# Kernel tuning notes

Measured on AMD Instinct MI355X. Metric: run time of the kernel, lower is better.

## Reference

```python
import jax, jax.numpy as jnp
import numpy as np

WS = 8          # window_size
HEADS = 6
DH = 32         # dim_head


def _dwconv(t, w):
    # t: (B,C,H,W), w: (C,1,3,3) depthwise, stride 1, padding 1 -> SAME
    return jax.lax.conv_general_dilated(
        t, w, window_strides=(1, 1), padding='SAME',
        feature_group_count=t.shape[1],
        dimension_numbers=('NCHW', 'OIHW', 'NCHW'))


def _l2norm(t, eps=1e-12):
    # matches F.normalize: x / max(||x||, eps)
    n = jnp.sqrt(jnp.sum(t * t, axis=-1, keepdims=True))
    return t / jnp.maximum(n, eps)


def setup_inputs() -> dict:
    key = jax.random.key(0)
    ks = jax.random.split(key, 10)
    B, H, W, C = 2, 256, 256, 192
    s = 0.05
    return {
        'x': jax.random.normal(ks[0], (B, H, W, C), jnp.float32),
        'illu_fea_trans': jax.random.normal(ks[1], (B, H, W, C), jnp.float32),
        'gt_w': jax.random.normal(ks[2], (C, C), jnp.float32) * s,
        'gt_b': jax.random.normal(ks[3], (C,), jnp.float32) * s,
        'qkv_w': jax.random.normal(ks[4], (C, 3 * C), jnp.float32) * s,
        'qkv_b': jax.random.normal(ks[5], (3 * C,), jnp.float32) * s,
        'proj_w': jax.random.normal(ks[6], (C, C), jnp.float32) * s,
        'proj_b': jax.random.normal(ks[7], (C,), jnp.float32) * s,
        'conv1_w': jax.random.normal(ks[8], (C, 1, 3, 3), jnp.float32) * s,
        'conv2_w': jax.random.normal(ks[9], (C, 1, 3, 3), jnp.float32) * s,
    }


def reference(x, illu_fea_trans, gt_w, gt_b, qkv_w, qkv_b, proj_w, proj_b,
              conv1_w, conv2_w):
    B, H, W, C = x.shape
    Ws, heads, d = WS, HEADS, DH
    scale = d ** (-0.5)
    pad_h = (Ws - H % Ws) % Ws
    pad_w = (Ws - W % Ws) % Ws
    xp = jnp.pad(x, ((0, 0), (0, pad_h), (0, pad_w), (0, 0)), mode='reflect')
    ip = jnp.pad(illu_fea_trans, ((0, 0), (0, pad_h), (0, pad_w), (0, 0)), mode='reflect')
    Hp, Wp = xp.shape[1], xp.shape[2]
    nW = (Hp // Ws) * (Wp // Ws)
    T = Ws * Ws

    def to_windows(t):
        t = t.reshape(B, Hp // Ws, Ws, Wp // Ws, Ws, C)
        return t.transpose(0, 1, 3, 2, 4, 5).reshape(B * nW, T, C)

    xw = to_windows(xp)                                  # (B*nW, T, C)
    qkv = (xw @ qkv_w + qkv_b).reshape(B * nW, T, 3, heads, d)
    qkv = qkv.transpose(2, 0, 3, 1, 4)                   # (3, Bn, h, T, d)
    q, k, v = qkv[0], qkv[1], qkv[2]
    q = _l2norm(q)
    k = _l2norm(k)

    illu = to_windows(ip).reshape(B * nW, T, heads, d).transpose(0, 2, 1, 3)
    v = v * (1.0 + jax.nn.sigmoid(illu))

    # global token: avg-pool over padded spatial dims, then linear
    gt = jnp.mean(xp, axis=(1, 2)) @ gt_w + gt_b          # (B, C)
    gt = gt.reshape(B, heads, 1, d)
    # faithful to torch expand(dim=2 -> nW).reshape(B*nW, heads, 1, d)
    gk = jnp.broadcast_to(gt, (B, heads, nW, d)).reshape(B * nW, heads, 1, d)
    k = jnp.concatenate([k, gk], axis=2)                  # (Bn, h, T+1, d)
    v = jnp.concatenate([v, gk], axis=2)

    # chunked softmax over keys == full softmax over key axis (chunks on q only)
    attn = jax.nn.softmax(jnp.einsum('bhqd,bhkd->bhqk', q, k) * scale, axis=-1)
    out = jnp.einsum('bhqk,bhkd->bhqd', attn, v)          # (Bn, h, T, d)
    out = out.transpose(0, 2, 1, 3).reshape(B * nW, T, C)
    out = out @ proj_w + proj_b

    out = out.reshape(B, Hp // Ws, Wp // Ws, Ws, Ws, C)
    out = out.transpose(0, 1, 3, 2, 4, 5).reshape(B, Hp, Wp, C)[:, :H, :W, :]

    # depthwise-conv positional branch on padded x (exact gelu like torch)
    t = xp.transpose(0, 3, 1, 2)                          # (B,C,Hp,Wp)
    t = _dwconv(t, conv1_w)
    t = jax.nn.gelu(t, approximate=False)
    t = _dwconv(t, conv2_w)
    pos = t.transpose(0, 2, 3, 1)[:, :H, :W, :]
    return out + pos
```

## Files before the change

### kernel.cpp

```cpp
#include <hip/hip_runtime.h>
#include <hip/hip_bf16.h>

#define BB   2
#define HH   256
#define WWD  256
#define CC   192
#define WSZ  8
#define TT   64
#define NHD  6
#define DHD  32
#define N3   576

typedef __attribute__((ext_vector_type(8))) short short8;
typedef __attribute__((ext_vector_type(4))) float f32x4;

__device__ inline short bf16_bits(float f) {
  __hip_bfloat16 h = __float2bfloat16(f);
  return __builtin_bit_cast(short, h);
}

__device__ inline float row_sum16(float v) {
  int x;
  x = __builtin_amdgcn_update_dpp(0, __builtin_bit_cast(int, v), 0xB1, 0xf, 0xf, true);
  v += __builtin_bit_cast(float, x);
  x = __builtin_amdgcn_update_dpp(0, __builtin_bit_cast(int, v), 0x4E, 0xf, 0xf, true);
  v += __builtin_bit_cast(float, x);
  x = __builtin_amdgcn_update_dpp(0, __builtin_bit_cast(int, v), 0x124, 0xf, 0xf, true);
  v += __builtin_bit_cast(float, x);
  x = __builtin_amdgcn_update_dpp(0, __builtin_bit_cast(int, v), 0x128, 0xf, 0xf, true);
  v += __builtin_bit_cast(float, x);
  return v;
}

__device__ inline void stage1k(const short* gsrc, short* ldst, int lane) {
  __builtin_amdgcn_global_load_lds(
      (const __attribute__((address_space(1))) void*)(gsrc + lane * 8),
      (__attribute__((address_space(3))) void*)ldst, 16, 0, 0);
}

__global__ __launch_bounds__(256) void lcam_wshuf2(const float* __restrict__ qkv_w,
                                                   const float* __restrict__ proj_w,
                                                   short* __restrict__ wf,
                                                   short* __restrict__ pwf) {
  int gid = blockIdx.x * 256 + threadIdx.x;
  const float* src; short* dst; int ncols, perm, g;
  if (gid < 13824) { src = qkv_w; dst = wf; ncols = N3; perm = 0; g = gid; }
  else {
    g = gid - 13824;
    if (g >= 4608) return;
    src = proj_w; dst = pwf; ncols = CC; perm = 1;
  }
  int lane = g & 63;
  int s = (g >> 6) % 6;
  int ct = g / 384;
  int col = ct * 16 + (lane & 15);
  int k0 = s * 32 + (lane >> 4) * 8;
  short8 v;
#pragma unroll
  for (int j = 0; j < 8; ++j)
    v[j] = bf16_bits(src[(size_t)(k0 + j) * ncols + col]);
  int didx = perm ? ((s * (ncols / 16) + ct) * 64 + lane) : g;
  *(short8*)(dst + (size_t)didx * 8) = v;
}

__global__ __launch_bounds__(192) void lcam_sum_x(const float* __restrict__ x,
                                                  float* __restrict__ sums) {
  int blk = blockIdx.x;
  int b = blk >> 9;
  int chunk = blk & 511;
  const float4* xp = (const float4*)(x + ((size_t)b * 65536 + (size_t)chunk * 128) * CC);
  int t = threadIdx.x;
  int pg = t / 48, c4 = t % 48;
  float4 acc = {0.f, 0.f, 0.f, 0.f};
  for (int p = 0; p < 32; ++p) {
    float4 v = xp[(size_t)(pg * 32 + p) * 48 + c4];
    acc.x += v.x; acc.y += v.y; acc.z += v.z; acc.w += v.w;
  }
  __shared__ __align__(16) float4 red[192];
  red[t] = acc;
  __syncthreads();
  if (pg == 0) {
    float4 a0 = red[c4], a1 = red[48 + c4], a2 = red[96 + c4], a3 = red[144 + c4];
    float* s = &sums[b * CC + c4 * 4];
    atomicAdd(s + 0, a0.x + a1.x + a2.x + a3.x);
    atomicAdd(s + 1, a0.y + a1.y + a2.y + a3.y);
    atomicAdd(s + 2, a0.z + a1.z + a2.z + a3.z);
    atomicAdd(s + 3, a0.w + a1.w + a2.w + a3.w);
  }
}

__global__ void lcam_gt(const float* __restrict__ sums,
                        const float* __restrict__ gt_w,
                        const float* __restrict__ gt_b,
                        float* __restrict__ gt) {
  int b = blockIdx.x;
  int co = threadIdx.x;
  float acc = gt_b[co];
  const float inv = 1.f / 65536.f;
  for (int c = 0; c < CC; ++c)
    acc += sums[b * CC + c] * inv * gt_w[c * CC + co];
  gt[b * CC + co] = acc;
}

__global__ __launch_bounds__(256) void lcam_attn(
    const float* __restrict__ x, const float* __restrict__ illu,
    const short* __restrict__ wf, const short* __restrict__ pwf,
    const float* __restrict__ qkv_b, const float* __restrict__ proj_b,
    const float* __restrict__ gt, float* __restrict__ out) {
  __shared__ __align__(16) short wgt[2][6144];
  __shared__ __align__(16) short ks[65 * 40];
  __shared__ __align__(16) short vt[32 * 72];
  __shared__ __align__(16) short qs[64 * 40];
  __shared__ __align__(16) short ps[64 * 72];

  int w = blockIdx.x;
  int b  = w >> 10;
  int wy = (w >> 5) & 31;
  int wx = w & 31;
  int t  = threadIdx.x;
  int lane = t & 63;
  int rtile = t >> 6;
  int m = lane & 15;
  int quad = lane >> 4;
  int key0 = rtile * 16 + quad * 4;

  size_t base = ((size_t)(b * HH + wy * WSZ) * WWD + wx * WSZ) * CC;

#pragma unroll
  for (int u = 0; u < 3; ++u) {
    int ii = rtile * 3 + u;
    stage1k(wf + ii * 512, wgt[0] + ii * 512, lane);
  }

  int apix = rtile * 16 + m;
  size_t arow = base + (size_t)((apix >> 3) * WWD + (apix & 7)) * CC + quad * 8;
  short8 afrag[6];
#pragma unroll
  for (int s = 0; s < 6; ++s) {
    const float* ap = x + arow + s * 32;
    float4 f0 = *(const float4*)(ap);
    float4 f1 = *(const float4*)(ap + 4);
    short8 v;
    v[0] = bf16_bits(f0.x); v[1] = bf16_bits(f0.y);
    v[2] = bf16_bits(f0.z); v[3] = bf16_bits(f0.w);
    v[4] = bf16_bits(f1.x); v[5] = bf16_bits(f1.y);
    v[6] = bf16_bits(f1.z); v[7] = bf16_bits(f1.w);
    afrag[s] = v;
  }

  float ila[NHD][4], ilb[NHD][4];
#pragma unroll
  for (int r = 0; r < 4; ++r) {
    int key = key0 + r;
    const float* ip = illu + base + (size_t)((key >> 3) * WWD + (key & 7)) * CC;
#pragma unroll
    for (int h = 0; h < NHD; ++h) {
      ila[h][r] = ip[h * 32 + m];
      ilb[h][r] = ip[h * 32 + 16 + m];
    }
  }

  const short8* wA8 = (const short8*)wgt[0];
  const short8* wB8 = (const short8*)wgt[1];

  f32x4 pacc[12];
#pragma unroll
  for (int ct = 0; ct < 12; ++ct) {
    f32x4 z = {0.f, 0.f, 0.f, 0.f};
    pacc[ct] = z;
  }

  __syncthreads();

#pragma unroll
  for (int h = 0; h < NHD; ++h) {
#pragma unroll
    for (int u = 0; u < 3; ++u) {
      int ii = rtile * 3 + u;
      stage1k(wf + (12 + 2 * h) * 3072 + ii * 512, wgt[1] + ii * 512, lane);
    }
    float gv0 = gt[b * CC + h * 32 + m];
    float gv1 = gt[b * CC + h * 32 + 16 + m];
    {
      f32x4 a0 = {0.f,0.f,0.f,0.f}, a1 = {0.f,0.f,0.f,0.f};
      __builtin_amdgcn_s_setprio(1);
#pragma unroll
      for (int s = 0; s < 6; ++s)
        a0 = __builtin_amdgcn_mfma_f32_16x16x32_bf16(afrag[s], wA8[s*64 + lane], a0, 0,0,0);
#pragma unroll
      for (int s = 0; s < 6; ++s)
        a1 = __builtin_amdgcn_mfma_f32_16x16x32_bf16(afrag[s], wA8[384 + s*64 + lane], a1, 0,0,0);
      __builtin_amdgcn_s_setprio(0);
      float b0 = qkv_b[h*32 + m], b1 = qkv_b[h*32 + 16 + m];
#pragma unroll
      for (int r = 0; r < 4; ++r) {
        float v0 = a0[r] + b0, v1 = a1[r] + b1;
        float ss = row_sum16(v0*v0 + v1*v1);
        float scl = 0.17677669529663688f * __builtin_amdgcn_rsqf(fmaxf(ss, 1e-24f));
        int row = key0 + r;
        qs[row*40 + m]      = bf16_bits(v0 * scl);
        qs[row*40 + 16 + m] = bf16_bits(v1 * scl);
      }
    }
    __syncthreads();
#pragma unroll
    for (int u = 0; u < 3; ++u) {
      int ii = rtile * 3 + u;
      stage1k(wf + (24 + 2 * h) * 3072 + ii * 512, wgt[0] + ii * 512, lane);
    }
    {
      f32x4 a0 = {0.f,0.f,0.f,0.f}, a1 = {0.f,0.f,0.f,0.f};
      __builtin_amdgcn_s_setprio(1);
#pragma unroll
      for (int s = 0; s < 6; ++s)
        a0 = __builtin_amdgcn_mfma_f32_16x16x32_bf16(afrag[s], wB8[s*64 + lane], a0, 0,0,0);
#pragma unroll
      for (int s = 0; s < 6; ++s)
        a1 = __builtin_amdgcn_mfma_f32_16x16x32_bf16(afrag[s], wB8[384 + s*64 + lane], a1, 0,0,0);
      __builtin_amdgcn_s_setprio(0);
      float b0 = qkv_b[192 + h*32 + m], b1 = qkv_b[192 + h*32 + 16 + m];
#pragma unroll
      for (int r = 0; r < 4; ++r) {
        float v0 = a0[r] + b0, v1 = a1[r] + b1;
        float ss = row_sum16(v0*v0 + v1*v1);
        float scl = __builtin_amdgcn_rsqf(fmaxf(ss, 1e-24f));
        int row = key0 + r;
        ks[row*40 + m]      = bf16_bits(v0 * scl);
        ks[row*40 + 16 + m] = bf16_bits(v1 * scl);
      }
    }
    __syncthreads();
#pragma unroll
    for (int u = 0; u < 3; ++u) {
      int ii = rtile * 3 + u;
      stage1k(pwf + h * 6144 + ii * 512, wgt[1] + ii * 512, lane);
    }
    {
      f32x4 a0 = {0.f,0.f,0.f,0.f}, a1 = {0.f,0.f,0.f,0.f};
      __builtin_amdgcn_s_setprio(1);
#pragma unroll
      for (int s = 0; s < 6; ++s)
        a0 = __builtin_amdgcn_mfma_f32_16x16x32_bf16(afrag[s], wA8[s*64 + lane], a0, 0,0,0);
#pragma unroll
      for (int s = 0; s < 6; ++s)
        a1 = __builtin_amdgcn_mfma_f32_16x16x32_bf16(afrag[s], wA8[384 + s*64 + lane], a1, 0,0,0);
      __builtin_amdgcn_s_setprio(0);
      float b0 = qkv_b[384 + h*32 + m], b1 = qkv_b[384 + h*32 + 16 + m];
#pragma unroll
      for (int r = 0; r < 4; ++r) {
        int key = key0 + r;
        float s0 = __builtin_amdgcn_rcpf(1.f + __expf(-ila[h][r]));
        float s1 = __builtin_amdgcn_rcpf(1.f + __expf(-ilb[h][r]));
        vt[m*72 + key]        = bf16_bits((a0[r] + b0) * (1.f + s0));
        vt[(16 + m)*72 + key] = bf16_bits((a1[r] + b1) * (1.f + s1));
      }
    }
    if (t < DHD) ks[64*40 + t] = bf16_bits(gt[b*CC + h*DHD + t]);
    __syncthreads();
    if (h < NHD - 1) {
#pragma unroll
      for (int u = 0; u < 3; ++u) {
        int ii = rtile * 3 + u;
        stage1k(wf + 2 * (h + 1) * 3072 + ii * 512, wgt[0] + ii * 512, lane);
      }
    }
    short8 qa = *(const short8*)(qs + (rtile*16 + m)*40 + quad*8);
    f32x4 sc[5];
#pragma unroll
    for (int ct = 0; ct < 4; ++ct) {
      short8 kb = *(const short8*)(ks + (ct*16 + m)*40 + quad*8);
      f32x4 z = {0.f,0.f,0.f,0.f};
      sc[ct] = __builtin_amdgcn_mfma_f32_16x16x32_bf16(qa, kb, z, 0,0,0);
    }
    {
      short8 kb = *(const short8*)(ks + 64*40 + quad*8);
      f32x4 z = {0.f,0.f,0.f,0.f};
      sc[4] = __builtin_amdgcn_mfma_f32_16x16x32_bf16(qa, kb, z, 0,0,0);
    }
    float p64v[4], invr[4];
#pragma unroll
    for (int r = 0; r < 4; ++r) {
      float e0 = __expf(sc[0][r]), e1 = __expf(sc[1][r]);
      float e2 = __expf(sc[2][r]), e3 = __expf(sc[3][r]);
      float e4 = __expf(sc[4][r]);
      int row = key0 + r;
      ps[row*72 + m]      = bf16_bits(e0);
      ps[row*72 + 16 + m] = bf16_bits(e1);
      ps[row*72 + 32 + m] = bf16_bits(e2);
      ps[row*72 + 48 + m] = bf16_bits(e3);
      float sum = row_sum16(e0 + e1 + e2 + e3) + e4;
      invr[r] = __builtin_amdgcn_rcpf(sum);
      p64v[r] = e4;
    }
    f32x4 o0 = {0.f,0.f,0.f,0.f}, o1 = {0.f,0.f,0.f,0.f};
    __builtin_amdgcn_s_setprio(1);
#pragma unroll
    for (int kc = 0; kc < 2; ++kc) {
      short8 pa  = *(const short8*)(ps + (rtile*16 + m)*72 + kc*32 + quad*8);
      short8 vb0 = *(const short8*)(vt + m*72        + kc*32 + quad*8);
      short8 vb1 = *(const short8*)(vt + (16 + m)*72 + kc*32 + quad*8);
      o0 = __builtin_amdgcn_mfma_f32_16x16x32_bf16(pa, vb0, o0, 0,0,0);
      o1 = __builtin_amdgcn_mfma_f32_16x16x32_bf16(pa, vb1, o1, 0,0,0);
    }
    __builtin_amdgcn_s_setprio(0);
#pragma unroll
    for (int r = 0; r < 4; ++r) {
      float pr = p64v[r];
      int row = key0 + r;
      qs[row*40 + m]      = bf16_bits((o0[r] + pr * gv0) * invr[r]);
      qs[row*40 + 16 + m] = bf16_bits((o1[r] + pr * gv1) * invr[r]);
    }
    short8 oa = *(const short8*)(qs + (rtile*16 + m)*40 + quad*8);
    __builtin_amdgcn_s_setprio(1);
#pragma unroll
    for (int ct = 0; ct < 12; ++ct)
      pacc[ct] = __builtin_amdgcn_mfma_f32_16x16x32_bf16(oa, wB8[ct*64 + lane], pacc[ct], 0,0,0);
    __builtin_amdgcn_s_setprio(0);
    __syncthreads();
  }
#pragma unroll
  for (int ct = 0; ct < 12; ++ct) {
    float bias = proj_b[ct*16 + m];
#pragma unroll
    for (int r = 0; r < 4; ++r) {
      int row = key0 + r;
      out[base + (size_t)((row >> 3) * WWD + (row & 7)) * CC + ct*16 + m] = pacc[ct][r] + bias;
    }
  }
}

__global__ __launch_bounds__(256) void lcam_pos(const float* __restrict__ x,
                                                const float* __restrict__ w1,
                                                const float* __restrict__ w2,
                                                float* __restrict__ out) {
  __shared__ __align__(16) float xt[20 * 20 * 16];
  __shared__ __align__(16) float t1[18 * 18 * 16];
  __shared__ float wl1[16 * 9], wl2[16 * 9];
  int blk = blockIdx.x;
  int cgI = blk % 12; int tmp = blk / 12;
  int tx = tmp % 16; tmp /= 16;
  int ty = tmp % 16; int b = tmp / 16;
  int c0 = cgI * 16;
  int y0 = ty * 16, x0 = tx * 16;
  int t = threadIdx.x;
  int cc4 = t & 3;
  if (t < 144) { wl1[t] = w1[c0 * 9 + t]; wl2[t] = w2[c0 * 9 + t]; }
  for (int vi = t; vi < 1600; vi += 256) {
    int q4 = vi & 3;
    int lin = vi >> 2;
    int xx = lin % 20, yy = lin / 20;
    int gy = y0 - 2 + yy, gx = x0 - 2 + xx;
    float4 v = {0.f, 0.f, 0.f, 0.f};
    if (gy >= 0 && gy < HH && gx >= 0 && gx < WWD)
      v = *(const float4*)(x + (((size_t)b * HH + gy) * WWD + gx) * CC + c0 + q4 * 4);
    *(float4*)(xt + (yy * 20 + xx) * 16 + q4 * 4) = v;
  }
  __syncthreads();
  float w1r[4][9], w2r[4][9];
#pragma unroll
  for (int j = 0; j < 4; ++j)
#pragma unroll
    for (int k = 0; k < 9; ++k) {
      w1r[j][k] = wl1[(cc4 * 4 + j) * 9 + k];
      w2r[j][k] = wl2[(cc4 * 4 + j) * 9 + k];
    }
  for (int idx = t; idx < 1296; idx += 256) {
    int lin = idx >> 2;
    int xx = lin % 18, yy = lin / 18;
    int gy = y0 - 1 + yy, gx = x0 - 1 + xx;
    float4 r = {0.f, 0.f, 0.f, 0.f};
    if (gy >= 0 && gy < HH && gx >= 0 && gx < WWD) {
#pragma unroll
      for (int ky = 0; ky < 3; ++ky)
#pragma unroll
        for (int kx = 0; kx < 3; ++kx) {
          float4 v = *(const float4*)(xt + ((yy + ky) * 20 + xx + kx) * 16 + cc4 * 4);
          int k = ky * 3 + kx;
          r.x += v.x * w1r[0][k];
          r.y += v.y * w1r[1][k];
          r.z += v.z * w1r[2][k];
          r.w += v.w * w1r[3][k];
        }
      r.x = 0.5f * r.x * (1.f + erff(r.x * 0.70710678118654752f));
      r.y = 0.5f * r.y * (1.f + erff(r.y * 0.70710678118654752f));
      r.z = 0.5f * r.z * (1.f + erff(r.z * 0.70710678118654752f));
      r.w = 0.5f * r.w * (1.f + erff(r.w * 0.70710678118654752f));
    }
    *(float4*)(t1 + (yy * 18 + xx) * 16 + cc4 * 4) = r;
  }
  __syncthreads();
  for (int idx = t; idx < 1024; idx += 256) {
    int lin = idx >> 2;
    int xx = lin & 15, yy = lin >> 4;
    float4 r = {0.f, 0.f, 0.f, 0.f};
#pragma unroll
    for (int ky = 0; ky < 3; ++ky)
#pragma unroll
      for (int kx = 0; kx < 3; ++kx) {
        float4 v = *(const float4*)(t1 + ((yy + ky) * 18 + xx + kx) * 16 + cc4 * 4);
        int k = ky * 3 + kx;
        r.x += v.x * w2r[0][k];
        r.y += v.y * w2r[1][k];
        r.z += v.z * w2r[2][k];
        r.w += v.w * w2r[3][k];
      }
    size_t o = (((size_t)b * HH + y0 + yy) * WWD + x0 + xx) * CC + c0 + cc4 * 4;
    float4 cur = *(float4*)(out + o);
    cur.x += r.x; cur.y += r.y; cur.z += r.z; cur.w += r.w;
    *(float4*)(out + o) = cur;
  }
}

extern "C" void kernel_launch(void* const* d_in, const int* in_sizes, int n_in,
                              void* d_out, int out_size, void* d_ws, size_t ws_size,
                              hipStream_t stream) {
  const float* x       = (const float*)d_in[0];
  const float* illu    = (const float*)d_in[1];
  const float* gt_w    = (const float*)d_in[2];
  const float* gt_b    = (const float*)d_in[3];
  const float* qkv_w   = (const float*)d_in[4];
  const float* qkv_b   = (const float*)d_in[5];
  const float* proj_w  = (const float*)d_in[6];
  const float* proj_b  = (const float*)d_in[7];
  const float* conv1_w = (const float*)d_in[8];
  const float* conv2_w = (const float*)d_in[9];
  float* out = (float*)d_out;

  short* wf   = (short*)d_ws;
  short* pwf  = (short*)((char*)d_ws + 221184);
  float* sums = (float*)((char*)d_ws + 221184 + 73728);
  float* gt   = sums + BB * CC;

  hipMemsetAsync(sums, 0, BB * CC * sizeof(float), stream);
  lcam_wshuf2<<<72, 256, 0, stream>>>(qkv_w, proj_w, wf, pwf);
  lcam_sum_x<<<1024, 192, 0, stream>>>(x, sums);
  lcam_gt<<<BB, CC, 0, stream>>>(sums, gt_w, gt_b, gt);
  lcam_attn<<<2048, 256, 0, stream>>>(x, illu, wf, pwf, qkv_b, proj_b, gt, out);
  lcam_pos<<<6144, 256, 0, stream>>>(x, conv1_w, conv2_w, out);
}
```

Before: 523.0 us.

## Process two windows per block, each wave handling two row tiles

Each 256-thread block now handles two attention windows instead of one. Each wave computes two 16-row tiles and reuses each weight fragment read from shared memory for two MFMAs. This halves the block count, and with it the number of times each block stages the full QKV and projection weights into LDS. It also halves the weight LDS reads per MFMA. The illumination loads move into the head loop. The cost is doubled accumulator registers (two sets of 12 projection accumulators plus the extra fragments), which could lower occupancy or cause spills. The per-window LDS buffers also double.

```diff
diff --git a/kernel.cpp b/kernel.cpp
--- a/kernel.cpp
+++ b/kernel.cpp
@@ -108,66 +108,69 @@
     const float* __restrict__ qkv_b, const float* __restrict__ proj_b,
     const float* __restrict__ gt, float* __restrict__ out) {
   __shared__ __align__(16) short wgt[2][6144];
-  __shared__ __align__(16) short ks[65 * 40];
-  __shared__ __align__(16) short vt[32 * 72];
-  __shared__ __align__(16) short qs[64 * 40];
-  __shared__ __align__(16) short ps[64 * 72];
-
-  int w = blockIdx.x;
-  int b  = w >> 10;
-  int wy = (w >> 5) & 31;
-  int wx = w & 31;
-  int t  = threadIdx.x;
+  __shared__ __align__(16) short ks[2][65 * 40];
+  __shared__ __align__(16) short vt[2][32 * 72];
+  __shared__ __align__(16) short qs[2][64 * 40];
+  __shared__ __align__(16) short ps[2][64 * 72];
+
+  int t = threadIdx.x;
   int lane = t & 63;
-  int rtile = t >> 6;
+  int wid = t >> 6;
+  int win = wid >> 1;
+  int half = wid & 1;
   int m = lane & 15;
   int quad = lane >> 4;
-  int key0 = rtile * 16 + quad * 4;
-
+  int tl = t & 127;
+
+  int wA = blockIdx.x * 2 + win;
+  int b  = wA >> 10;
+  int wy = (wA >> 5) & 31;
+  int wx = wA & 31;
   size_t base = ((size_t)(b * HH + wy * WSZ) * WWD + wx * WSZ) * CC;
 
+  short* ksb = ks[win];
+  short* vtb = vt[win];
+  short* qsb = qs[win];
+  short* psb = ps[win];
+
+  int rb0 = half * 32;
+  int rb1 = half * 32 + 16;
+  int key00 = rb0 + quad * 4;
+  int key01 = rb1 + quad * 4;
+
 #pragma unroll
   for (int u = 0; u < 3; ++u) {
-    int ii = rtile * 3 + u;
+    int ii = wid * 3 + u;
     stage1k(wf + ii * 512, wgt[0] + ii * 512, lane);
   }
 
-  int apix = rtile * 16 + m;
-  size_t arow = base + (size_t)((apix >> 3) * WWD + (apix & 7)) * CC + quad * 8;
-  short8 afrag[6];
-#pragma unroll
-  for (int s = 0; s < 6; ++s) {
-    const float* ap = x + arow + s * 32;
-    float4 f0 = *(const float4*)(ap);
-    float4 f1 = *(const float4*)(ap + 4);
-    short8 v;
-    v[0] = bf16_bits(f0.x); v[1] = bf16_bits(f0.y);
-    v[2] = bf16_bits(f0.z); v[3] = bf16_bits(f0.w);
-    v[4] = bf16_bits(f1.x); v[5] = bf16_bits(f1.y);
-    v[6] = bf16_bits(f1.z); v[7] = bf16_bits(f1.w);
-    afrag[s] = v;
-  }
-
-  float ila[NHD][4], ilb[NHD][4];
-#pragma unroll
-  for (int r = 0; r < 4; ++r) {
-    int key = key0 + r;
-    const float* ip = illu + base + (size_t)((key >> 3) * WWD + (key & 7)) * CC;
-#pragma unroll
-    for (int h = 0; h < NHD; ++h) {
-      ila[h][r] = ip[h * 32 + m];
-      ilb[h][r] = ip[h * 32 + 16 + m];
+  short8 af0[6], af1[6];
+#pragma unroll
+  for (int g = 0; g < 2; ++g) {
+    int apix = (g ? rb1 : rb0) + m;
+    size_t arow = base + (size_t)((apix >> 3) * WWD + (apix & 7)) * CC + quad * 8;
+#pragma unroll
+    for (int s = 0; s < 6; ++s) {
+      const float* ap = x + arow + s * 32;
+      float4 f0 = *(const float4*)(ap);
+      float4 f1 = *(const float4*)(ap + 4);
+      short8 v;
+      v[0] = bf16_bits(f0.x); v[1] = bf16_bits(f0.y);
+      v[2] = bf16_bits(f0.z); v[3] = bf16_bits(f0.w);
+      v[4] = bf16_bits(f1.x); v[5] = bf16_bits(f1.y);
+      v[6] = bf16_bits(f1.z); v[7] = bf16_bits(f1.w);
+      if (g) af1[s] = v; else af0[s] = v;
     }
   }
 
   const short8* wA8 = (const short8*)wgt[0];
   const short8* wB8 = (const short8*)wgt[1];
 
-  f32x4 pacc[12];
+  f32x4 pacc0[12], pacc1[12];
 #pragma unroll
   for (int ct = 0; ct < 12; ++ct) {
     f32x4 z = {0.f, 0.f, 0.f, 0.f};
-    pacc[ct] = z;
+    pacc0[ct] = z; pacc1[ct] = z;
   }
 
   __syncthreads();
@@ -176,145 +179,215 @@
   for (int h = 0; h < NHD; ++h) {
 #pragma unroll
     for (int u = 0; u < 3; ++u) {
-      int ii = rtile * 3 + u;
+      int ii = wid * 3 + u;
       stage1k(wf + (12 + 2 * h) * 3072 + ii * 512, wgt[1] + ii * 512, lane);
     }
     float gv0 = gt[b * CC + h * 32 + m];
     float gv1 = gt[b * CC + h * 32 + 16 + m];
+    float il00[4], il01[4], il10[4], il11[4];
+#pragma unroll
+    for (int r = 0; r < 4; ++r) {
+      int k0r = key00 + r, k1r = key01 + r;
+      const float* ip0 = illu + base + (size_t)((k0r >> 3) * WWD + (k0r & 7)) * CC + h * 32;
+      const float* ip1 = illu + base + (size_t)((k1r >> 3) * WWD + (k1r & 7)) * CC + h * 32;
+      il00[r] = ip0[m]; il01[r] = ip0[16 + m];
+      il10[r] = ip1[m]; il11[r] = ip1[16 + m];
+    }
     {
-      f32x4 a0 = {0.f,0.f,0.f,0.f}, a1 = {0.f,0.f,0.f,0.f};
+      f32x4 a00 = {0.f,0.f,0.f,0.f}, a01 = {0.f,0.f,0.f,0.f};
+      f32x4 a10 = {0.f,0.f,0.f,0.f}, a11 = {0.f,0.f,0.f,0.f};
       __builtin_amdgcn_s_setprio(1);
 #pragma unroll
-      for (int s = 0; s < 6; ++s)
-        a0 = __builtin_amdgcn_mfma_f32_16x16x32_bf16(afrag[s], wA8[s*64 + lane], a0, 0,0,0);
-#pragma unroll
-      for (int s = 0; s < 6; ++s)
-        a1 = __builtin_amdgcn_mfma_f32_16x16x32_bf16(afrag[s], wA8[384 + s*64 + lane], a1, 0,0,0);
+      for (int s = 0; s < 6; ++s) {
+        short8 w0 = wA8[s*64 + lane];
+        a00 = __builtin_amdgcn_mfma_f32_16x16x32_bf16(af0[s], w0, a00, 0,0,0);
+        a10 = __builtin_amdgcn_mfma_f32_16x16x32_bf16(af1[s], w0, a10, 0,0,0);
+      }
+#pragma unroll
+      for (int s = 0; s < 6; ++s) {
+        short8 w1 = wA8[384 + s*64 + lane];
+        a01 = __builtin_amdgcn_mfma_f32_16x16x32_bf16(af0[s], w1, a01, 0,0,0);
+        a11 = __builtin_amdgcn_mfma_f32_16x16x32_bf16(af1[s], w1, a11, 0,0,0);
+      }
       __builtin_amdgcn_s_setprio(0);
       float b0 = qkv_b[h*32 + m], b1 = qkv_b[h*32 + 16 + m];
 #pragma unroll
       for (int r = 0; r < 4; ++r) {
-        float v0 = a0[r] + b0, v1 = a1[r] + b1;
+        float v0 = a00[r] + b0, v1 = a01[r] + b1;
         float ss = row_sum16(v0*v0 + v1*v1);
         float scl = 0.17677669529663688f * __builtin_amdgcn_rsqf(fmaxf(ss, 1e-24f));
-        int row = key0 + r;
-        qs[row*40 + m]      = bf16_bits(v0 * scl);
-        qs[row*40 + 16 + m] = bf16_bits(v1 * scl);
+        int row = key00 + r;
+        qsb[row*40 + m]      = bf16_bits(v0 * scl);
+        qsb[row*40 + 16 + m] = bf16_bits(v1 * scl);
+        float w0 = a10[r] + b0, w1 = a11[r] + b1;
+        float ss1 = row_sum16(w0*w0 + w1*w1);
+        float scl1 = 0.17677669529663688f * __builtin_amdgcn_rsqf(fmaxf(ss1, 1e-24f));
+        int row1 = key01 + r;
+        qsb[row1*40 + m]      = bf16_bits(w0 * scl1);
+        qsb[row1*40 + 16 + m] = bf16_bits(w1 * scl1);
       }
     }
     __syncthreads();
 #pragma unroll
     for (int u = 0; u < 3; ++u) {
-      int ii = rtile * 3 + u;
+      int ii = wid * 3 + u;
       stage1k(wf + (24 + 2 * h) * 3072 + ii * 512, wgt[0] + ii * 512, lane);
     }
     {
-      f32x4 a0 = {0.f,0.f,0.f,0.f}, a1 = {0.f,0.f,0.f,0.f};
+      f32x4 a00 = {0.f,0.f,0.f,0.f}, a01 = {0.f,0.f,0.f,0.f};
+      f32x4 a10 = {0.f,0.f,0.f,0.f}, a11 = {0.f,0.f,0.f,0.f};
       __builtin_amdgcn_s_setprio(1);
 #pragma unroll
-      for (int s = 0; s < 6; ++s)
-        a0 = __builtin_amdgcn_mfma_f32_16x16x32_bf16(afrag[s], wB8[s*64 + lane], a0, 0,0,0);
-#pragma unroll
-      for (int s = 0; s < 6; ++s)
-        a1 = __builtin_amdgcn_mfma_f32_16x16x32_bf16(afrag[s], wB8[384 + s*64 + lane], a1, 0,0,0);
+      for (int s = 0; s < 6; ++s) {
+        short8 w0 = wB8[s*64 + lane];
+        a00 = __builtin_amdgcn_mfma_f32_16x16x32_bf16(af0[s], w0, a00, 0,0,0);
+        a10 = __builtin_amdgcn_mfma_f32_16x16x32_bf16(af1[s], w0, a10, 0,0,0);
+      }
+#pragma unroll
+      for (int s = 0; s < 6; ++s) {
+        short8 w1 = wB8[384 + s*64 + lane];
+        a01 = __builtin_amdgcn_mfma_f32_16x16x32_bf16(af0[s], w1, a01, 0,0,0);
+        a11 = __builtin_amdgcn_mfma_f32_16x16x32_bf16(af1[s], w1, a11, 0,0,0);
+      }
       __builtin_amdgcn_s_setprio(0);
       float b0 = qkv_b[192 + h*32 + m], b1 = qkv_b[192 + h*32 + 16 + m];
 #pragma unroll
       for (int r = 0; r < 4; ++r) {
-        float v0 = a0[r] + b0, v1 = a1[r] + b1;
+        float v0 = a00[r] + b0, v1 = a01[r] + b1;
         float ss = row_sum16(v0*v0 + v1*v1);
         float scl = __builtin_amdgcn_rsqf(fmaxf(ss, 1e-24f));
-        int row = key0 + r;
-        ks[row*40 + m]      = bf16_bits(v0 * scl);
-        ks[row*40 + 16 + m] = bf16_bits(v1 * scl);
+        int row = key00 + r;
+        ksb[row*40 + m]      = bf16_bits(v0 * scl);
+        ksb[row*40 + 16 + m] = bf16_bits(v1 * scl);
+        float w0 = a10[r] + b0, w1 = a11[r] + b1;
+        float ss1 = row_sum16(w0*w0 + w1*w1);
+        float scl1 = __builtin_amdgcn_rsqf(fmaxf(ss1, 1e-24f));
+        int row1 = key01 + r;
+        ksb[row1*40 + m]      = bf16_bits(w0 * scl1);
+        ksb[row1*40 + 16 + m] = bf16_bits(w1 * scl1);
       }
     }
     __syncthreads();
 #pragma unroll
     for (int u = 0; u < 3; ++u) {
-      int ii = rtile * 3 + u;
+      int ii = wid * 3 + u;
       stage1k(pwf + h * 6144 + ii * 512, wgt[1] + ii * 512, lane);
     }
     {
-      f32x4 a0 = {0.f,0.f,0.f,0.f}, a1 = {0.f,0.f,0.f,0.f};
+      f32x4 a00 = {0.f,0.f,0.f,0.f}, a01 = {0.f,0.f,0.f,0.f};
+      f32x4 a10 = {0.f,0.f,0.f,0.f}, a11 = {0.f,0.f,0.f,0.f};
       __builtin_amdgcn_s_setprio(1);
 #pragma unroll
-      for (int s = 0; s < 6; ++s)
-        a0 = __builtin_amdgcn_mfma_f32_16x16x32_bf16(afrag[s], wA8[s*64 + lane], a0, 0,0,0);
-#pragma unroll
-      for (int s = 0; s < 6; ++s)
-        a1 = __builtin_amdgcn_mfma_f32_16x16x32_bf16(afrag[s], wA8[384 + s*64 + lane], a1, 0,0,0);
+      for (int s = 0; s < 6; ++s) {
+        short8 w0 = wA8[s*64 + lane];
+        a00 = __builtin_amdgcn_mfma_f32_16x16x32_bf16(af0[s], w0, a00, 0,0,0);
+        a10 = __builtin_amdgcn_mfma_f32_16x16x32_bf16(af1[s], w0, a10, 0,0,0);
+      }
+#pragma unroll
+      for (int s = 0; s < 6; ++s) {
+        short8 w1 = wA8[384 + s*64 + lane];
+        a01 = __builtin_amdgcn_mfma_f32_16x16x32_bf16(af0[s], w1, a01, 0,0,0);
+        a11 = __builtin_amdgcn_mfma_f32_16x16x32_bf16(af1[s], w1, a11, 0,0,0);
+      }
       __builtin_amdgcn_s_setprio(0);
       float b0 = qkv_b[384 + h*32 + m], b1 = qkv_b[384 + h*32 + 16 + m];
 #pragma unroll
       for (int r = 0; r < 4; ++r) {
-        int key = key0 + r;
-        float s0 = __builtin_amdgcn_rcpf(1.f + __expf(-ila[h][r]));
-        float s1 = __builtin_amdgcn_rcpf(1.f + __expf(-ilb[h][r]));
-        vt[m*72 + key]        = bf16_bits((a0[r] + b0) * (1.f + s0));
-        vt[(16 + m)*72 + key] = bf16_bits((a1[r] + b1) * (1.f + s1));
-      }
-    }
-    if (t < DHD) ks[64*40 + t] = bf16_bits(gt[b*CC + h*DHD + t]);
+        int k0r = key00 + r, k1r = key01 + r;
+        float s00 = __builtin_amdgcn_rcpf(1.f + __expf(-il00[r]));
+        float s01 = __builtin_amdgcn_rcpf(1.f + __expf(-il01[r]));
+        float s10 = __builtin_amdgcn_rcpf(1.f + __expf(-il10[r]));
+        float s11 = __builtin_amdgcn_rcpf(1.f + __expf(-il11[r]));
+        vtb[m*72 + k0r]        = bf16_bits((a00[r] + b0) * (1.f + s00));
+        vtb[(16 + m)*72 + k0r] = bf16_bits((a01[r] + b1) * (1.f + s01));
+        vtb[m*72 + k1r]        = bf16_bits((a10[r] + b0) * (1.f + s10));
+        vtb[(16 + m)*72 + k1r] = bf16_bits((a11[r] + b1) * (1.f + s11));
+      }
+    }
+    if (tl < DHD) ksb[64*40 + tl] = bf16_bits(gt[b*CC + h*DHD + tl]);
     __syncthreads();
     if (h < NHD - 1) {
 #pragma unroll
       for (int u = 0; u < 3; ++u) {
-        int ii = rtile * 3 + u;
+        int ii = wid * 3 + u;
         stage1k(wf + 2 * (h + 1) * 3072 + ii * 512, wgt[0] + ii * 512, lane);
       }
     }
-    short8 qa = *(const short8*)(qs + (rtile*16 + m)*40 + quad*8);
-    f32x4 sc[5];
+    short8 qa0 = *(const short8*)(qsb + (rb0 + m)*40 + quad*8);
+    short8 qa1 = *(const short8*)(qsb + (rb1 + m)*40 + quad*8);
+    f32x4 sc0[5], sc1[5];
+    __builtin_amdgcn_s_setprio(1);
 #pragma unroll
     for (int ct = 0; ct < 4; ++ct) {
-      short8 kb = *(const short8*)(ks + (ct*16 + m)*40 + quad*8);
+      short8 kb = *(const short8*)(ksb + (ct*16 + m)*40 + quad*8);
       f32x4 z = {0.f,0.f,0.f,0.f};
-      sc[ct] = __builtin_amdgcn_mfma_f32_16x16x32_bf16(qa, kb, z, 0,0,0);
+      sc0[ct] = __builtin_amdgcn_mfma_f32_16x16x32_bf16(qa0, kb, z, 0,0,0);
+      sc1[ct] = __builtin_amdgcn_mfma_f32_16x16x32_bf16(qa1, kb, z, 0,0,0);
     }
     {
-      short8 kb = *(const short8*)(ks + 64*40 + quad*8);
+      short8 kb = *(const short8*)(ksb + 64*40 + quad*8);
       f32x4 z = {0.f,0.f,0.f,0.f};
-      sc[4] = __builtin_amdgcn_mfma_f32_16x16x32_bf16(qa, kb, z, 0,0,0);
-    }
-    float p64v[4], invr[4];
+      sc0[4] = __builtin_amdgcn_mfma_f32_16x16x32_bf16(qa0, kb, z, 0,0,0);
+      sc1[4] = __builtin_amdgcn_mfma_f32_16x16x32_bf16(qa1, kb, z, 0,0,0);
+    }
+    __builtin_amdgcn_s_setprio(0);
+    float p640[4], inv0[4], p641[4], inv1[4];
 #pragma unroll
     for (int r = 0; r < 4; ++r) {
-      float e0 = __expf(sc[0][r]), e1 = __expf(sc[1][r]);
-      float e2 = __expf(sc[2][r]), e3 = __expf(sc[3][r]);
-      float e4 = __expf(sc[4][r]);
-      int row = key0 + r;
-      ps[row*72 + m]      = bf16_bits(e0);
-      ps[row*72 + 16 + m] = bf16_bits(e1);
-      ps[row*72 + 32 + m] = bf16_bits(e2);
-      ps[row*72 + 48 + m] = bf16_bits(e3);
-      float sum = row_sum16(e0 + e1 + e2 + e3) + e4;
-      invr[r] = __builtin_amdgcn_rcpf(sum);
-      p64v[r] = e4;
-    }
-    f32x4 o0 = {0.f,0.f,0.f,0.f}, o1 = {0.f,0.f,0.f,0.f};
+      float e0 = __expf(sc0[0][r]), e1 = __expf(sc0[1][r]);
+      float e2 = __expf(sc0[2][r]), e3 = __expf(sc0[3][r]);
+      float e4 = __expf(sc0[4][r]);
+      int row = key00 + r;
+      psb[row*72 + m]      = bf16_bits(e0);
+      psb[row*72 + 16 + m] = bf16_bits(e1);
+      psb[row*72 + 32 + m] = bf16_bits(e2);
+      psb[row*72 + 48 + m] = bf16_bits(e3);
+      inv0[r] = __builtin_amdgcn_rcpf(row_sum16(e0 + e1 + e2 + e3) + e4);
+      p640[r] = e4;
+      float f0 = __expf(sc1[0][r]), f1 = __expf(sc1[1][r]);
+      float f2 = __expf(sc1[2][r]), f3 = __expf(sc1[3][r]);
+      float f4 = __expf(sc1[4][r]);
+      int row1 = key01 + r;
+      psb[row1*72 + m]      = bf16_bits(f0);
+      psb[row1*72 + 16 + m] = bf16_bits(f1);
+      psb[row1*72 + 32 + m] = bf16_bits(f2);
+      psb[row1*72 + 48 + m] = bf16_bits(f3);
+      inv1[r] = __builtin_amdgcn_rcpf(row_sum16(f0 + f1 + f2 + f3) + f4);
+      p641[r] = f4;
+    }
+    f32x4 o00 = {0.f,0.f,0.f,0.f}, o01 = {0.f,0.f,0.f,0.f};
+    f32x4 o10 = {0.f,0.f,0.f,0.f}, o11 = {0.f,0.f,0.f,0.f};
     __builtin_amdgcn_s_setprio(1);
 #pragma unroll
     for (int kc = 0; kc < 2; ++kc) {
-      short8 pa  = *(const short8*)(ps + (rtile*16 + m)*72 + kc*32 + quad*8);
-      short8 vb0 = *(const short8*)(vt + m*72        + kc*32 + quad*8);
-      short8 vb1 = *(const short8*)(vt + (16 + m)*72 + kc*32 + quad*8);
-      o0 = __builtin_amdgcn_mfma_f32_16x16x32_bf16(pa, vb0, o0, 0,0,0);
-      o1 = __builtin_amdgcn_mfma_f32_16x16x32_bf16(pa, vb1, o1, 0,0,0);
+      short8 pa0 = *(const short8*)(psb + (rb0 + m)*72 + kc*32 + quad*8);
+      short8 pa1 = *(const short8*)(psb + (rb1 + m)*72 + kc*32 + quad*8);
+      short8 vb0 = *(const short8*)(vtb + m*72        + kc*32 + quad*8);
+      short8 vb1 = *(const short8*)(vtb + (16 + m)*72 + kc*32 + quad*8);
+      o00 = __builtin_amdgcn_mfma_f32_16x16x32_bf16(pa0, vb0, o00, 0,0,0);
+      o01 = __builtin_amdgcn_mfma_f32_16x16x32_bf16(pa0, vb1, o01, 0,0,0);
+      o10 = __builtin_amdgcn_mfma_f32_16x16x32_bf16(pa1, vb0, o10, 0,0,0);
+      o11 = __builtin_amdgcn_mfma_f32_16x16x32_bf16(pa1, vb1, o11, 0,0,0);
     }
     __builtin_amdgcn_s_setprio(0);
 #pragma unroll
     for (int r = 0; r < 4; ++r) {
-      float pr = p64v[r];
-      int row = key0 + r;
-      qs[row*40 + m]      = bf16_bits((o0[r] + pr * gv0) * invr[r]);
-      qs[row*40 + 16 + m] = bf16_bits((o1[r] + pr * gv1) * invr[r]);
-    }
-    short8 oa = *(const short8*)(qs + (rtile*16 + m)*40 + quad*8);
+      int row = key00 + r;
+      qsb[row*40 + m]      = bf16_bits((o00[r] + p640[r] * gv0) * inv0[r]);
+      qsb[row*40 + 16 + m] = bf16_bits((o01[r] + p640[r] * gv1) * inv0[r]);
+      int row1 = key01 + r;
+      qsb[row1*40 + m]      = bf16_bits((o10[r] + p641[r] * gv0) * inv1[r]);
+      qsb[row1*40 + 16 + m] = bf16_bits((o11[r] + p641[r] * gv1) * inv1[r]);
+    }
+    short8 oa0 = *(const short8*)(qsb + (rb0 + m)*40 + quad*8);
+    short8 oa1 = *(const short8*)(qsb + (rb1 + m)*40 + quad*8);
     __builtin_amdgcn_s_setprio(1);
 #pragma unroll
-    for (int ct = 0; ct < 12; ++ct)
-      pacc[ct] = __builtin_amdgcn_mfma_f32_16x16x32_bf16(oa, wB8[ct*64 + lane], pacc[ct], 0,0,0);
+    for (int ct = 0; ct < 12; ++ct) {
+      short8 wfrag = wB8[ct*64 + lane];
+      pacc0[ct] = __builtin_amdgcn_mfma_f32_16x16x32_bf16(oa0, wfrag, pacc0[ct], 0,0,0);
+      pacc1[ct] = __builtin_amdgcn_mfma_f32_16x16x32_bf16(oa1, wfrag, pacc1[ct], 0,0,0);
+    }
     __builtin_amdgcn_s_setprio(0);
     __syncthreads();
   }
@@ -323,8 +396,10 @@
     float bias = proj_b[ct*16 + m];
 #pragma unroll
     for (int r = 0; r < 4; ++r) {
-      int row = key0 + r;
-      out[base + (size_t)((row >> 3) * WWD + (row & 7)) * CC + ct*16 + m] = pacc[ct][r] + bias;
+      int row = key00 + r;
+      out[base + (size_t)((row >> 3) * WWD + (row & 7)) * CC + ct*16 + m] = pacc0[ct][r] + bias;
+      int row1 = key01 + r;
+      out[base + (size_t)((row1 >> 3) * WWD + (row1 & 7)) * CC + ct*16 + m] = pacc1[ct][r] + bias;
     }
   }
 }
@@ -435,6 +510,6 @@
   lcam_wshuf2<<<72, 256, 0, stream>>>(qkv_w, proj_w, wf, pwf);
   lcam_sum_x<<<1024, 192, 0, stream>>>(x, sums);
   lcam_gt<<<BB, CC, 0, stream>>>(sums, gt_w, gt_b, gt);
-  lcam_attn<<<2048, 256, 0, stream>>>(x, illu, wf, pwf, qkv_b, proj_b, gt, out);
+  lcam_attn<<<1024, 256, 0, stream>>>(x, illu, wf, pwf, qkv_b, proj_b, gt, out);
   lcam_pos<<<6144, 256, 0, stream>>>(x, conv1_w, conv2_w, out);
 }
```

Result: slower. 550.8 us (+5.3%).
